# Performance work log

Hardware: AMD Instinct MI355X
Metric: run time of the kernel (lower is better)

Reference implementation:

```python
import jax, jax.numpy as jnp
import numpy as np

B = 32768
D_IN = 512
D_OUT = 512
N_DIGITS = 9
N_LEVELS = N_DIGITS + 1


def _xavier_uniform(key, shape, gain):
    # nn.init.xavier_uniform_ on Linear weight of shape (out, in)
    fan_out, fan_in = shape
    limit = gain * np.sqrt(6.0 / (fan_in + fan_out))
    return jax.random.uniform(key, shape, jnp.float32, -limit, limit)


def setup_inputs() -> dict:
    key = jax.random.key(0)
    kx, kv, *kw = jax.random.split(key, 2 + N_LEVELS)
    x = jax.random.normal(kx, (B, D_IN), dtype=jnp.float32)
    valuations = jax.random.randint(kv, (B,), 0, N_LEVELS, dtype=jnp.int64)
    # level-aware xavier init: gain = 1/(1 + 0.1*level)
    W = jnp.stack([
        _xavier_uniform(kw[l], (D_OUT, D_IN), 1.0 / (1.0 + 0.1 * l))
        for l in range(N_LEVELS)
    ], axis=0)  # (L, out, in)
    level_gates = jnp.ones((N_LEVELS,), dtype=jnp.float32)
    cross_level_attn = (jnp.eye(N_LEVELS, dtype=jnp.float32) * 0.9
                        + jnp.ones((N_LEVELS, N_LEVELS), dtype=jnp.float32) * 0.01)
    bias = jnp.zeros((D_OUT,), dtype=jnp.float32)
    return {"x": x, "valuations": valuations, "W": W,
            "level_gates": level_gates, "cross_level_attn": cross_level_attn,
            "bias": bias}


def reference(x, valuations, W, level_gates, cross_level_attn, bias):
    val = jnp.clip(valuations, 0, N_DIGITS)  # (B,)
    # 10 per-level linears as one batched GEMM: (B, L, out)
    level_outputs = jnp.einsum('bi,loi->blo', x, W)
    gates = jax.nn.sigmoid(level_gates)  # (L,)
    level_outputs = level_outputs * gates[None, :, None]
    # per-sample gather of own valuation level -> (B, out)
    output = jnp.take_along_axis(level_outputs, val[:, None, None], axis=1)[:, 0, :]
    # soft cross-level attention combine
    attn_weights = jax.nn.softmax(cross_level_attn[val], axis=-1)  # (B, L)
    weighted = jnp.einsum('bl,blo->bo', attn_weights, level_outputs)
    output = 0.7 * output + 0.3 * weighted
    return output + bias
```

## Files before the change

### kernel.cpp

```cpp
#include <hip/hip_runtime.h>

#define B_N 32768
#define D 512
#define DD (D * D)
#define NLEV 10
#define TM 128
#define TN 256
#define BK 32
#define NITER (D / BK)
#define NHB 128
#define MROWS_MAX 34048
#define MAX_RT (MROWS_MAX / TM)

typedef unsigned short u16;
typedef short s16x8 __attribute__((ext_vector_type(8)));
typedef u16 u16x8 __attribute__((ext_vector_type(8)));
typedef float f32x4 __attribute__((ext_vector_type(4)));

__device__ __forceinline__ u16 f2bf(float f) {
  union { float f; unsigned u; } v; v.f = f;
  unsigned r = v.u + 0x7fffu + ((v.u >> 16) & 1u);
  return (u16)(r >> 16);
}
__device__ __forceinline__ int clampv(int v) {
  return v < 0 ? 0 : (v > NLEV - 1 ? NLEV - 1 : v);
}

__global__ void k1(const float* __restrict__ W, const float* __restrict__ lg,
                   const float* __restrict__ attn, const int* __restrict__ val,
                   u16* __restrict__ weff, u16* __restrict__ hist,
                   int* __restrict__ perm) {
  const int t = threadIdx.x;
  if (blockIdx.x < DD / 256) {
    __shared__ float c[NLEV * NLEV];
    if (t < NLEV) {
      float g[NLEV], a[NLEV], mx = -1e30f;
      #pragma unroll
      for (int l = 0; l < NLEV; ++l) {
        g[l] = 1.0f / (1.0f + expf(-lg[l]));
        a[l] = attn[t * NLEV + l];
        mx = fmaxf(mx, a[l]);
      }
      float s = 0.f;
      #pragma unroll
      for (int l = 0; l < NLEV; ++l) { a[l] = expf(a[l] - mx); s += a[l]; }
      float inv = 1.0f / s;
      #pragma unroll
      for (int l = 0; l < NLEV; ++l) {
        float cc = 0.3f * a[l] * inv * g[l];
        if (l == t) cc += 0.7f * g[t];
        c[t * NLEV + l] = cc;
      }
    }
    __syncthreads();
    const int idx = blockIdx.x * 256 + t;
    float w[NLEV];
    #pragma unroll
    for (int l = 0; l < NLEV; ++l) w[l] = W[l * DD + idx];
    #pragma unroll
    for (int v = 0; v < NLEV; ++v) {
      float s = 0.f;
      #pragma unroll
      for (int l = 0; l < NLEV; ++l) s += c[v * NLEV + l] * w[l];
      weff[v * DD + idx] = f2bf(s);
    }
  } else {
    __shared__ int lc[NLEV];
    const int b = blockIdx.x - DD / 256;
    if (t < NLEV) lc[t] = 0;
    __syncthreads();
    const int gid = b * 256 + t;
    atomicAdd(&lc[clampv(val[gid])], 1);
    perm[gid] = -1;
    if (b < (MROWS_MAX - B_N) / 256) perm[B_N + b * 256 + t] = -1;
    __syncthreads();
    if (t < NLEV) hist[b * NLEV + t] = (u16)lc[t];
  }
}

__global__ void k2(const int* __restrict__ val, const u16* __restrict__ hist,
                   int* __restrict__ perm, int* __restrict__ starts) {
  __shared__ int h[NHB * NLEV];
  __shared__ int st[NLEV + 1];
  __shared__ int cnt[NLEV];
  __shared__ int lc[NLEV];
  const int t = threadIdx.x, b = blockIdx.x;
  for (int i = t; i < NHB * NLEV; i += 256) h[i] = hist[i];
  if (t < NLEV) lc[t] = 0;
  __syncthreads();
  if (t < NLEV) {
    int run = 0;
    for (int bb = 0; bb < NHB; ++bb) {
      int x = h[bb * NLEV + t];
      h[bb * NLEV + t] = run;
      run += x;
    }
    cnt[t] = run;
  }
  __syncthreads();
  if (t == 0) {
    int s = 0;
    for (int v = 0; v < NLEV; ++v) {
      st[v] = s;
      s += (cnt[v] + TM - 1) & ~(TM - 1);
    }
    st[NLEV] = s;
  }
  __syncthreads();
  const int gid = b * 256 + t;
  const int v = clampv(val[gid]);
  const int pos = atomicAdd(&lc[v], 1);
  perm[st[v] + h[b * NLEV + v] + pos] = gid;
  if (b == 0 && t <= NLEV) starts[t] = st[t];
}

__global__ __launch_bounds__(512, 4) void k3(
    const float* __restrict__ x, const u16* __restrict__ weff,
    const int* __restrict__ perm, const int* __restrict__ starts,
    const float* __restrict__ bias, float* __restrict__ out) {
  __shared__ float Asf[2][TM * BK];
  __shared__ u16   Bsu[2][TN * BK];

  const int ct = blockIdx.x, rt = blockIdx.y;
  const int Mpad = starts[NLEV];
  if (rt * TM >= Mpad) return;

  int v = 0;
  #pragma unroll
  for (int i = 1; i < NLEV; ++i) if (rt * TM >= starts[i]) v = i;

  const int tid = threadIdx.x;
  const int lane = tid & 63, wave = tid >> 6;
  const int wm = (wave >> 2) * 64, wn = (wave & 3) * 64;
  const int fm = lane & 15;
  const int cb = lane >> 4;

  const int arow = tid >> 3;
  const int kch = (tid & 7) ^ (arow & 7);
  int pr0 = perm[rt * TM + arow];
  int pr1 = perm[rt * TM + 64 + arow];
  if (pr0 < 0) pr0 = 0;
  if (pr1 < 0) pr1 = 0;
  const float* ga0 = x + (size_t)pr0 * D + kch * 4;
  const float* ga1 = x + (size_t)pr1 * D + kch * 4;
  const int adst0 = tid * 4;
  const int adst1 = (512 + tid) * 4;

  const u16* wb = weff + ((size_t)v * D + ct * TN) * D;
  const int c0i = wave * 64 + lane;
  const int c1i = 512 + c0i;
  const int n0 = c0i >> 2, s0 = c0i & 3, kc0 = s0 ^ ((n0 >> 1) & 3);
  const int n1 = c1i >> 2, s1 = c1i & 3, kc1 = s1 ^ ((n1 >> 1) & 3);
  const u16* gb0 = wb + n0 * D + kc0 * 8;
  const u16* gb1 = wb + n1 * D + kc1 * 8;
  const int bdst0 = c0i * 8, bdst1 = c1i * 8;

  const int sl0 = (2 * cb) ^ (fm & 7);
  const int sl1 = (2 * cb + 1) ^ (fm & 7);

  f32x4 acc[4][4];
  #pragma unroll
  for (int i = 0; i < 4; ++i)
    #pragma unroll
    for (int j = 0; j < 4; ++j) acc[i][j] = (f32x4){0.f, 0.f, 0.f, 0.f};

  __builtin_amdgcn_global_load_lds(
      (const __attribute__((address_space(1))) void*)ga0,
      (__attribute__((address_space(3))) void*)(Asf[0] + adst0), 16, 0, 0);
  __builtin_amdgcn_global_load_lds(
      (const __attribute__((address_space(1))) void*)ga1,
      (__attribute__((address_space(3))) void*)(Asf[0] + adst1), 16, 0, 0);
  __builtin_amdgcn_global_load_lds(
      (const __attribute__((address_space(1))) void*)gb0,
      (__attribute__((address_space(3))) void*)(Bsu[0] + bdst0), 16, 0, 0);
  __builtin_amdgcn_global_load_lds(
      (const __attribute__((address_space(1))) void*)gb1,
      (__attribute__((address_space(3))) void*)(Bsu[0] + bdst1), 16, 0, 0);
  asm volatile("s_waitcnt vmcnt(0)" ::: "memory");
  __builtin_amdgcn_s_barrier();
  __builtin_amdgcn_sched_barrier(0);

  int p = 0;
  for (int i = 0; i < NITER; ++i) {
    const bool hn = (i + 1 < NITER);
    if (hn) {
      const int ko = (i + 1) * BK;
      __builtin_amdgcn_global_load_lds(
          (const __attribute__((address_space(1))) void*)(ga0 + ko),
          (__attribute__((address_space(3))) void*)(Asf[p ^ 1] + adst0), 16, 0, 0);
      __builtin_amdgcn_global_load_lds(
          (const __attribute__((address_space(1))) void*)(ga1 + ko),
          (__attribute__((address_space(3))) void*)(Asf[p ^ 1] + adst1), 16, 0, 0);
      __builtin_amdgcn_global_load_lds(
          (const __attribute__((address_space(1))) void*)(gb0 + ko),
          (__attribute__((address_space(3))) void*)(Bsu[p ^ 1] + bdst0), 16, 0, 0);
      __builtin_amdgcn_global_load_lds(
          (const __attribute__((address_space(1))) void*)(gb1 + ko),
          (__attribute__((address_space(3))) void*)(Bsu[p ^ 1] + bdst1), 16, 0, 0);
    }
    const float* Af = (const float*)Asf[p];
    s16x8 af[4], bf[4];
    #pragma unroll
    for (int t4 = 0; t4 < 4; ++t4) {
      const int m = wm + t4 * 16 + fm;
      const f32x4 lo = *(const f32x4*)(Af + m * 32 + sl0 * 4);
      const f32x4 hi = *(const f32x4*)(Af + m * 32 + sl1 * 4);
      union { unsigned w[4]; s16x8 v; } u;
      asm("v_cvt_pk_bf16_f32 %0, %1, %2" : "=v"(u.w[0]) : "v"(lo[0]), "v"(lo[1]));
      asm("v_cvt_pk_bf16_f32 %0, %1, %2" : "=v"(u.w[1]) : "v"(lo[2]), "v"(lo[3]));
      asm("v_cvt_pk_bf16_f32 %0, %1, %2" : "=v"(u.w[2]) : "v"(hi[0]), "v"(hi[1]));
      asm("v_cvt_pk_bf16_f32 %0, %1, %2" : "=v"(u.w[3]) : "v"(hi[2]), "v"(hi[3]));
      af[t4] = u.v;
      const int n = wn + t4 * 16 + fm;
      bf[t4] = *(const s16x8*)(Bsu[p] + n * BK + ((cb ^ ((n >> 1) & 3)) << 3));
    }
    __builtin_amdgcn_s_setprio(1);
    #pragma unroll
    for (int tm = 0; tm < 4; ++tm)
      #pragma unroll
      for (int tn = 0; tn < 4; ++tn)
        acc[tm][tn] = __builtin_amdgcn_mfma_f32_16x16x32_bf16(af[tm], bf[tn], acc[tm][tn], 0, 0, 0);
    __builtin_amdgcn_s_setprio(0);
    if (hn) {
      asm volatile("s_waitcnt vmcnt(0)" ::: "memory");
      asm volatile("s_waitcnt lgkmcnt(0)" ::: "memory");
      __builtin_amdgcn_s_barrier();
      __builtin_amdgcn_sched_barrier(0);
    }
    p ^= 1;
  }

  float bv[4];
  #pragma unroll
  for (int tn = 0; tn < 4; ++tn) bv[tn] = bias[ct * TN + wn + tn * 16 + fm];
  #pragma unroll
  for (int tm = 0; tm < 4; ++tm) {
    #pragma unroll
    for (int r = 0; r < 4; ++r) {
      const int mrow = wm + tm * 16 + (lane >> 4) * 4 + r;
      const int p2 = perm[rt * TM + mrow];
      if (p2 >= 0) {
        float* o = out + (size_t)p2 * D + ct * TN + wn + fm;
        #pragma unroll
        for (int tn = 0; tn < 4; ++tn)
          o[tn * 16] = acc[tm][tn][r] + bv[tn];
      }
    }
  }
}

extern "C" void kernel_launch(void* const* d_in, const int* in_sizes, int n_in,
                              void* d_out, int out_size, void* d_ws, size_t ws_size,
                              hipStream_t stream) {
  const float* x    = (const float*)d_in[0];
  const int*   val  = (const int*)d_in[1];
  const float* W    = (const float*)d_in[2];
  const float* lg   = (const float*)d_in[3];
  const float* attn = (const float*)d_in[4];
  const float* bias = (const float*)d_in[5];
  float* out = (float*)d_out;

  char* ws = (char*)d_ws;
  int* starts = (int*)(ws + 0);
  u16* hist   = (u16*)(ws + 64);
  int* perm   = (int*)(ws + 2688);
  u16* weff   = (u16*)(ws + 139264);

  k1<<<DD / 256 + NHB, 256, 0, stream>>>(W, lg, attn, val, weff, hist, perm);
  k2<<<NHB, 256, 0, stream>>>(val, hist, perm, starts);
  k3<<<dim3(D / TN, MAX_RT), 512, 0, stream>>>(x, weff, perm, starts, bias, out);
}
```

Before: 177.6 us.

## Convert staged fp32 A tile to bf16 once into a swizzled LDS buffer

```diff
diff --git a/kernel.cpp b/kernel.cpp
--- a/kernel.cpp
+++ b/kernel.cpp
@@ -16,6 +16,7 @@
 typedef short s16x8 __attribute__((ext_vector_type(8)));
 typedef u16 u16x8 __attribute__((ext_vector_type(8)));
 typedef float f32x4 __attribute__((ext_vector_type(4)));
+typedef unsigned u32x2 __attribute__((ext_vector_type(2)));
 
 __device__ __forceinline__ u16 f2bf(float f) {
   union { float f; unsigned u; } v; v.f = f;
@@ -118,7 +119,8 @@
     const float* __restrict__ x, const u16* __restrict__ weff,
     const int* __restrict__ perm, const int* __restrict__ starts,
     const float* __restrict__ bias, float* __restrict__ out) {
-  __shared__ float Asf[2][TM * BK];
+  __shared__ float Xs[2][TM * BK];
+  __shared__ u16   Abf[2][TM * BK];
   __shared__ u16   Bsu[2][TN * BK];
 
   const int ct = blockIdx.x, rt = blockIdx.y;
@@ -136,15 +138,19 @@
   const int cb = lane >> 4;
 
   const int arow = tid >> 3;
-  const int kch = (tid & 7) ^ (arow & 7);
+  const int aq   = tid & 7;
   int pr0 = perm[rt * TM + arow];
   int pr1 = perm[rt * TM + 64 + arow];
   if (pr0 < 0) pr0 = 0;
   if (pr1 < 0) pr1 = 0;
-  const float* ga0 = x + (size_t)pr0 * D + kch * 4;
-  const float* ga1 = x + (size_t)pr1 * D + kch * 4;
-  const int adst0 = tid * 4;
-  const int adst1 = (512 + tid) * 4;
+  const float* ga0 = x + (size_t)pr0 * D + aq * 4;
+  const float* ga1 = x + (size_t)pr1 * D + aq * 4;
+  const int ad0 = tid * 4;
+  const int ad1 = (512 + tid) * 4;
+
+  const int csl = (aq >> 1) ^ ((arow >> 1) & 3);
+  const int co0 = arow * 32 + csl * 8 + (aq & 1) * 4;
+  const int co1 = (64 + arow) * 32 + csl * 8 + (aq & 1) * 4;
 
   const u16* wb = weff + ((size_t)v * D + ct * TN) * D;
   const int c0i = wave * 64 + lane;
@@ -155,28 +161,37 @@
   const u16* gb1 = wb + n1 * D + kc1 * 8;
   const int bdst0 = c0i * 8, bdst1 = c1i * 8;
 
-  const int sl0 = (2 * cb) ^ (fm & 7);
-  const int sl1 = (2 * cb + 1) ^ (fm & 7);
-
   f32x4 acc[4][4];
   #pragma unroll
   for (int i = 0; i < 4; ++i)
     #pragma unroll
     for (int j = 0; j < 4; ++j) acc[i][j] = (f32x4){0.f, 0.f, 0.f, 0.f};
 
-  __builtin_amdgcn_global_load_lds(
-      (const __attribute__((address_space(1))) void*)ga0,
-      (__attribute__((address_space(3))) void*)(Asf[0] + adst0), 16, 0, 0);
-  __builtin_amdgcn_global_load_lds(
-      (const __attribute__((address_space(1))) void*)ga1,
-      (__attribute__((address_space(3))) void*)(Asf[0] + adst1), 16, 0, 0);
   __builtin_amdgcn_global_load_lds(
       (const __attribute__((address_space(1))) void*)gb0,
       (__attribute__((address_space(3))) void*)(Bsu[0] + bdst0), 16, 0, 0);
   __builtin_amdgcn_global_load_lds(
       (const __attribute__((address_space(1))) void*)gb1,
       (__attribute__((address_space(3))) void*)(Bsu[0] + bdst1), 16, 0, 0);
+  __builtin_amdgcn_global_load_lds(
+      (const __attribute__((address_space(1))) void*)ga0,
+      (__attribute__((address_space(3))) void*)(Xs[0] + ad0), 16, 0, 0);
+  __builtin_amdgcn_global_load_lds(
+      (const __attribute__((address_space(1))) void*)ga1,
+      (__attribute__((address_space(3))) void*)(Xs[0] + ad1), 16, 0, 0);
   asm volatile("s_waitcnt vmcnt(0)" ::: "memory");
+  {
+    const f32x4 c0 = *(const f32x4*)(Xs[0] + ad0);
+    const f32x4 c1 = *(const f32x4*)(Xs[0] + ad1);
+    unsigned w0, w1, w2, w3;
+    asm("v_cvt_pk_bf16_f32 %0, %1, %2" : "=v"(w0) : "v"(c0[0]), "v"(c0[1]));
+    asm("v_cvt_pk_bf16_f32 %0, %1, %2" : "=v"(w1) : "v"(c0[2]), "v"(c0[3]));
+    asm("v_cvt_pk_bf16_f32 %0, %1, %2" : "=v"(w2) : "v"(c1[0]), "v"(c1[1]));
+    asm("v_cvt_pk_bf16_f32 %0, %1, %2" : "=v"(w3) : "v"(c1[2]), "v"(c1[3]));
+    *(u32x2*)(Abf[0] + co0) = (u32x2){w0, w1};
+    *(u32x2*)(Abf[0] + co1) = (u32x2){w2, w3};
+  }
+  asm volatile("s_waitcnt lgkmcnt(0)" ::: "memory");
   __builtin_amdgcn_s_barrier();
   __builtin_amdgcn_sched_barrier(0);
 
@@ -186,31 +201,23 @@
     if (hn) {
       const int ko = (i + 1) * BK;
       __builtin_amdgcn_global_load_lds(
-          (const __attribute__((address_space(1))) void*)(ga0 + ko),
-          (__attribute__((address_space(3))) void*)(Asf[p ^ 1] + adst0), 16, 0, 0);
-      __builtin_amdgcn_global_load_lds(
-          (const __attribute__((address_space(1))) void*)(ga1 + ko),
-          (__attribute__((address_space(3))) void*)(Asf[p ^ 1] + adst1), 16, 0, 0);
-      __builtin_amdgcn_global_load_lds(
           (const __attribute__((address_space(1))) void*)(gb0 + ko),
           (__attribute__((address_space(3))) void*)(Bsu[p ^ 1] + bdst0), 16, 0, 0);
       __builtin_amdgcn_global_load_lds(
           (const __attribute__((address_space(1))) void*)(gb1 + ko),
           (__attribute__((address_space(3))) void*)(Bsu[p ^ 1] + bdst1), 16, 0, 0);
-    }
-    const float* Af = (const float*)Asf[p];
+      __builtin_amdgcn_global_load_lds(
+          (const __attribute__((address_space(1))) void*)(ga0 + ko),
+          (__attribute__((address_space(3))) void*)(Xs[p ^ 1] + ad0), 16, 0, 0);
+      __builtin_amdgcn_global_load_lds(
+          (const __attribute__((address_space(1))) void*)(ga1 + ko),
+          (__attribute__((address_space(3))) void*)(Xs[p ^ 1] + ad1), 16, 0, 0);
+    }
     s16x8 af[4], bf[4];
     #pragma unroll
     for (int t4 = 0; t4 < 4; ++t4) {
       const int m = wm + t4 * 16 + fm;
-      const f32x4 lo = *(const f32x4*)(Af + m * 32 + sl0 * 4);
-      const f32x4 hi = *(const f32x4*)(Af + m * 32 + sl1 * 4);
-      union { unsigned w[4]; s16x8 v; } u;
-      asm("v_cvt_pk_bf16_f32 %0, %1, %2" : "=v"(u.w[0]) : "v"(lo[0]), "v"(lo[1]));
-      asm("v_cvt_pk_bf16_f32 %0, %1, %2" : "=v"(u.w[1]) : "v"(lo[2]), "v"(lo[3]));
-      asm("v_cvt_pk_bf16_f32 %0, %1, %2" : "=v"(u.w[2]) : "v"(hi[0]), "v"(hi[1]));
-      asm("v_cvt_pk_bf16_f32 %0, %1, %2" : "=v"(u.w[3]) : "v"(hi[2]), "v"(hi[3]));
-      af[t4] = u.v;
+      af[t4] = *(const s16x8*)(Abf[p] + m * BK + ((cb ^ ((m >> 1) & 3)) << 3));
       const int n = wn + t4 * 16 + fm;
       bf[t4] = *(const s16x8*)(Bsu[p] + n * BK + ((cb ^ ((n >> 1) & 3)) << 3));
     }
@@ -223,6 +230,15 @@
     __builtin_amdgcn_s_setprio(0);
     if (hn) {
       asm volatile("s_waitcnt vmcnt(0)" ::: "memory");
+      const f32x4 c0 = *(const f32x4*)(Xs[p ^ 1] + ad0);
+      const f32x4 c1 = *(const f32x4*)(Xs[p ^ 1] + ad1);
+      unsigned w0, w1, w2, w3;
+      asm("v_cvt_pk_bf16_f32 %0, %1, %2" : "=v"(w0) : "v"(c0[0]), "v"(c0[1]));
+      asm("v_cvt_pk_bf16_f32 %0, %1, %2" : "=v"(w1) : "v"(c0[2]), "v"(c0[3]));
+      asm("v_cvt_pk_bf16_f32 %0, %1, %2" : "=v"(w2) : "v"(c1[0]), "v"(c1[1]));
+      asm("v_cvt_pk_bf16_f32 %0, %1, %2" : "=v"(w3) : "v"(c1[2]), "v"(c1[3]));
+      *(u32x2*)(Abf[p ^ 1] + co0) = (u32x2){w0, w1};
+      *(u32x2*)(Abf[p ^ 1] + co1) = (u32x2){w2, w3};
       asm volatile("s_waitcnt lgkmcnt(0)" ::: "memory");
       __builtin_amdgcn_s_barrier();
       __builtin_amdgcn_sched_barrier(0);
```

Result: faster. 173.3 us (-2.4%).
